# Optimization experiments

Measured on AMD Instinct MI355X. Metric: run time of the kernel, lower is better.

The kernel has to match this reference:

```python
import jax, jax.numpy as jnp
import numpy as np

B, S, D, K, NS = 4, 2048, 768, 8192, 2
TAU = 1.0


def setup_inputs() -> dict:
    key = jax.random.key(0)
    k1, k2, k3, k4 = jax.random.split(key, 4)
    x = jax.random.normal(k1, (B, S, D), dtype=jnp.float32)
    w_codebook = jax.random.normal(k2, (K, D), dtype=jnp.float32) * (1.0 / np.sqrt(D))
    embeddings = jax.random.normal(k3, (K, D), dtype=jnp.float32)
    # standard Gumbel(0,1) noise, one draw per (token, sample, code)
    gumbel_noise = jax.random.gumbel(k4, (B, S, NS, K), dtype=jnp.float32)
    return {"x": x, "w_codebook": w_codebook, "embeddings": embeddings,
            "gumbel_noise": gumbel_noise, "num_samples": NS}


def reference(x, w_codebook, embeddings, gumbel_noise, num_samples):
    # logits = Linear(x) without bias: [B, S, K]
    logits = jnp.einsum('bsd,kd->bsk', x, w_codebook)
    # expand over num_samples and add Gumbel noise (F.gumbel_softmax, training)
    g = (logits[:, :, None, :] + gumbel_noise) / TAU          # [B, S, NS, K]
    y_soft = jax.nn.softmax(g, axis=-1)
    # hard one-hot with straight-through estimator (hard=True, hard_p=1.0)
    idx = jnp.argmax(y_soft, axis=-1)                          # [B, S, NS]
    y_hard = jax.nn.one_hot(idx, K, dtype=y_soft.dtype)
    indices = y_hard + y_soft - jax.lax.stop_gradient(y_soft)  # [B, S, NS, K]
    # one-hot matmul == gather of codebook rows
    emb = jnp.einsum('bsnk,kd->bsnd', indices, embeddings)     # [B, S, NS, D]
    return emb, indices
```

## Files before the change

### kernel.cpp

```cpp
#include <hip/hip_runtime.h>
#include <stdint.h>

#define Bc 4
#define Sc 2048
#define Dc 768
#define Kc 8192
#define NSc 2
#define Mc (Bc*Sc)
#define EMB_ELEMS ((size_t)Mc*NSc*Dc)

typedef __attribute__((ext_vector_type(8))) __bf16 bf16x8;
typedef __attribute__((ext_vector_type(4))) float f32x4;
typedef __attribute__((ext_vector_type(4))) unsigned short u16x4;
typedef __attribute__((ext_vector_type(8))) unsigned short u16x8;

__device__ __forceinline__ unsigned short f2bf(float f){
  unsigned int u = __float_as_uint(f);
  u += 0x7FFFu + ((u >> 16) & 1u);
  return (unsigned short)(u >> 16);
}
__device__ __forceinline__ float bf2f(unsigned short h){
  return __uint_as_float(((unsigned int)h) << 16);
}

__global__ __launch_bounds__(256) void k_convert(const float4* __restrict__ x,
                                                 const float4* __restrict__ w,
                                                 u16x4* __restrict__ xb,
                                                 u16x4* __restrict__ wb){
  int i = blockIdx.x * 256 + threadIdx.x;
  float4 v = x[i];
  u16x4 o;
  o.x = f2bf(v.x); o.y = f2bf(v.y); o.z = f2bf(v.z); o.w = f2bf(v.w);
  xb[i] = o;
  v = w[i];
  o.x = f2bf(v.x); o.y = f2bf(v.y); o.z = f2bf(v.z); o.w = f2bf(v.w);
  wb[i] = o;
}

#define BM 128
#define BN 128
#define BK 32

__global__ __launch_bounds__(512, 2) void k_gemm(const unsigned short* __restrict__ xb,
                                                 const unsigned short* __restrict__ wb,
                                                 unsigned short* __restrict__ stash){
  __shared__ __align__(16) unsigned char lds[131072];

  const int tid  = threadIdx.x;
  const int lane = tid & 63;
  const int wid  = tid >> 6;
  const int wr   = wid >> 2;
  const int wc   = wid & 3;
  const int fr   = lane & 15;
  const int fq   = lane >> 4;

  const int bid = (int)blockIdx.x;
  const int xcd = bid & 7;
  const int ii  = bid >> 3;
  const int bm0 = (ii >> 2) * 256;
  const int bn0 = (xcd * 4 + (ii & 3)) * 256;

  f32x4 acc[8][4] = {};

  const int rin   = tid >> 3;
  const int kblkp = (tid & 7) ^ (rin & 7);
  const unsigned short* gsrc[8];
  unsigned dstoff[8];
  #pragma unroll
  for (int s = 0; s < 8; ++s) {
    const int isA = s >> 2;
    const int q   = s & 3;
    const int r64 = isA ? (((q & 1) << 1) | (q >> 1)) : q;
    const int grow = (isA ? bm0 : bn0) + r64 * 64 + rin;
    gsrc[s]   = (isA ? xb : wb) + (size_t)grow * Dc + kblkp * 8;
    dstoff[s] = (isA ? 0u : 32768u) + (unsigned)r64 * 8192u + (unsigned)wid * 1024u;
  }

#define ISSUE(s_, bo_) __builtin_amdgcn_global_load_lds( \
    (const __attribute__((address_space(1))) void*)gsrc[s_], \
    (__attribute__((address_space(3))) void*)&lds[(bo_) + dstoff[s_]], 16, 0, 0)

  #pragma unroll
  for (int s = 0; s < 8; ++s) ISSUE(s, 0u);
  #pragma unroll
  for (int s = 0; s < 8; ++s) gsrc[s] += 64;

  unsigned bufR = 0u, bufW = 65536u;
  const unsigned aRow = (unsigned)(wr*128 + fr) * 128u;
  const unsigned bRow = (unsigned)(wc*64  + fr) * 128u + 32768u;
  const unsigned sl0  = (unsigned)((fq       ) ^ (fr & 7)) * 16u;
  const unsigned sl1  = (unsigned)((fq + 4   ) ^ (fr & 7)) * 16u;

  for (int t = 0; t < 12; ++t) {
    const bool more = (t < 11);
    bf16x8 a[4], b0[4], b1[4];

    asm volatile("s_waitcnt vmcnt(2)" ::: "memory");
    __builtin_amdgcn_s_barrier();
    asm volatile("" ::: "memory");
    if (more) { ISSUE(0, bufW); ISSUE(1, bufW); }
    #pragma unroll
    for (int n = 0; n < 4; ++n) b0[n] = *(const bf16x8*)&lds[bufR + bRow + (unsigned)n*2048u + sl0];
    #pragma unroll
    for (int m = 0; m < 4; ++m) a[m]  = *(const bf16x8*)&lds[bufR + aRow + (unsigned)m*2048u + sl0];
    __builtin_amdgcn_s_setprio(1);
    #pragma unroll
    for (int m = 0; m < 4; ++m)
      #pragma unroll
      for (int n = 0; n < 4; ++n)
        acc[m][n] = __builtin_amdgcn_mfma_f32_16x16x32_bf16(a[m], b0[n], acc[m][n], 0, 0, 0);
    __builtin_amdgcn_s_setprio(0);

    if (more) asm volatile("s_waitcnt vmcnt(2)" ::: "memory");
    else      asm volatile("s_waitcnt vmcnt(0)" ::: "memory");
    __builtin_amdgcn_s_barrier();
    asm volatile("" ::: "memory");
    if (more) { ISSUE(2, bufW); ISSUE(3, bufW); }
    #pragma unroll
    for (int m = 0; m < 4; ++m) a[m] = *(const bf16x8*)&lds[bufR + aRow + 8192u + (unsigned)m*2048u + sl0];
    __builtin_amdgcn_s_setprio(1);
    #pragma unroll
    for (int m = 0; m < 4; ++m)
      #pragma unroll
      for (int n = 0; n < 4; ++n)
        acc[4+m][n] = __builtin_amdgcn_mfma_f32_16x16x32_bf16(a[m], b0[n], acc[4+m][n], 0, 0, 0);
    __builtin_amdgcn_s_setprio(0);

    if (more) { ISSUE(4, bufW); ISSUE(5, bufW); }
    #pragma unroll
    for (int n = 0; n < 4; ++n) b1[n] = *(const bf16x8*)&lds[bufR + bRow + (unsigned)n*2048u + sl1];
    #pragma unroll
    for (int m = 0; m < 4; ++m) a[m]  = *(const bf16x8*)&lds[bufR + aRow + (unsigned)m*2048u + sl1];
    __builtin_amdgcn_s_setprio(1);
    #pragma unroll
    for (int m = 0; m < 4; ++m)
      #pragma unroll
      for (int n = 0; n < 4; ++n)
        acc[m][n] = __builtin_amdgcn_mfma_f32_16x16x32_bf16(a[m], b1[n], acc[m][n], 0, 0, 0);
    __builtin_amdgcn_s_setprio(0);

    if (more) { ISSUE(6, bufW); ISSUE(7, bufW); }
    #pragma unroll
    for (int m = 0; m < 4; ++m) a[m] = *(const bf16x8*)&lds[bufR + aRow + 8192u + (unsigned)m*2048u + sl1];
    __builtin_amdgcn_s_setprio(1);
    #pragma unroll
    for (int m = 0; m < 4; ++m)
      #pragma unroll
      for (int n = 0; n < 4; ++n)
        acc[4+m][n] = __builtin_amdgcn_mfma_f32_16x16x32_bf16(a[m], b1[n], acc[4+m][n], 0, 0, 0);
    __builtin_amdgcn_s_setprio(0);

    bufR ^= 65536u; bufW ^= 65536u;
    if (t < 10) {
      #pragma unroll
      for (int s = 0; s < 8; ++s) gsrc[s] += 64;
    }
  }
#undef ISSUE

  unsigned short* tb16 = (unsigned short*)lds;
  #pragma unroll
  for (int h = 0; h < 2; ++h) {
    __syncthreads();
    if (wr == h) {
      #pragma unroll
      for (int m = 0; m < 8; ++m)
        #pragma unroll
        for (int n = 0; n < 4; ++n)
          #pragma unroll
          for (int r = 0; r < 4; ++r)
            tb16[(m*16 + fq*4 + r)*264 + (wc*64 + n*16 + fr)] = f2bf(acc[m][n][r]);
    }
    __syncthreads();
    #pragma unroll
    for (int i = 0; i < 8; ++i) {
      const int n = i*512 + tid;
      const int row = n >> 5, seg = n & 31;
      *(u16x8*)&stash[(size_t)(bm0 + h*128 + row) * 32768 + bn0 + seg*8] =
          *(const u16x8*)&tb16[row*264 + seg*8];
    }
  }
}

#define MARGIN 0.125f

__global__ __launch_bounds__(256) void k_select(const unsigned short* logits,
                                                const float* __restrict__ gumbel,
                                                const float* __restrict__ x,
                                                const float* __restrict__ w,
                                                const float* __restrict__ emb_tab,
                                                float* __restrict__ out_emb,
                                                float* out_ind){
  const int t   = blockIdx.x;
  const int tid = threadIdx.x;
  const int lane = tid & 63, wid = tid >> 6;

  __shared__ unsigned short Lrow[Kc];
  __shared__ float wmax[4];
  __shared__ int   cand_k[16];
  __shared__ float cand_g[16];
  __shared__ int   cand_cnt;
  __shared__ int   sel_idx[NSc];

  {
    const u16x4* src = (const u16x4*)(logits + (size_t)t * 32768);
    u16x4* dst = (u16x4*)Lrow;
    #pragma unroll
    for (int j = 0; j < 8; j++) dst[j*256 + tid] = src[j*256 + tid];
  }
  __syncthreads();

  for (int s = 0; s < NSc; ++s) {
    const float* grow = gumbel + ((size_t)t * NSc + s) * Kc;
    float4 vals[8];
    float m = -1e30f;
    #pragma unroll
    for (int j = 0; j < 8; j++) {
      float4 g4 = ((const float4*)grow)[j*256 + tid];
      u16x4 l4 = *(const u16x4*)&Lrow[j*1024 + tid*4];
      float4 v;
      v.x = bf2f(l4.x) + g4.x;
      v.y = bf2f(l4.y) + g4.y;
      v.z = bf2f(l4.z) + g4.z;
      v.w = bf2f(l4.w) + g4.w;
      vals[j] = v;
      m = fmaxf(m, fmaxf(fmaxf(v.x, v.y), fmaxf(v.z, v.w)));
    }
    #pragma unroll
    for (int off = 32; off; off >>= 1) m = fmaxf(m, __shfl_xor(m, off));
    if (lane == 0) wmax[wid] = m;
    __syncthreads();
    const float gmax = fmaxf(fmaxf(wmax[0], wmax[1]), fmaxf(wmax[2], wmax[3]));
    if (tid == 0) cand_cnt = 0;
    __syncthreads();

    const float thr = gmax - MARGIN;
    #pragma unroll
    for (int j = 0; j < 8; j++) {
      const int k0 = j*1024 + tid*4;
      float vv[4] = {vals[j].x, vals[j].y, vals[j].z, vals[j].w};
      #pragma unroll
      for (int q = 0; q < 4; q++) {
        if (vv[q] >= thr) {
          int p = atomicAdd(&cand_cnt, 1);
          if (p < 16) cand_k[p] = k0 + q;
        }
      }
    }
    __syncthreads();

    const int cnt = min(cand_cnt, 16);
    int idx;
    if (cnt == 1) {
      idx = cand_k[0];
    } else {
      for (int c = wid; c < cnt; c += 4) {
        const int kc = cand_k[c];
        const float* wr = w + (size_t)kc * Dc;
        const float* xr = x + (size_t)t * Dc;
        double accd = 0.0;
        for (int d = lane; d < Dc; d += 64) accd += (double)xr[d] * (double)wr[d];
        #pragma unroll
        for (int off = 32; off; off >>= 1) accd += __shfl_xor(accd, off);
        if (lane == 0) cand_g[c] = (float)accd + grow[kc];
      }
      __syncthreads();
      if (tid == 0) {
        float bg = -1e30f; int bk_ = Kc;
        for (int c = 0; c < cnt; c++) {
          float g = cand_g[c]; int kk = cand_k[c];
          if (g > bg || (g == bg && kk < bk_)) { bg = g; bk_ = kk; }
        }
        sel_idx[s] = bk_;
      }
      __syncthreads();
      idx = sel_idx[s];
    }
    if (cnt == 1 && tid == 0) sel_idx[s] = idx;
    __syncthreads();

    float* irow = out_ind + ((size_t)t * NSc + s) * Kc;
    #pragma unroll
    for (int j = 0; j < 8; j++) {
      const int k0 = j*1024 + tid*4;
      float4 z = {0.f, 0.f, 0.f, 0.f};
      const int d = sel_idx[s] - k0;
      if (d == 0) z.x = 1.0f; else if (d == 1) z.y = 1.0f;
      else if (d == 2) z.z = 1.0f; else if (d == 3) z.w = 1.0f;
      ((float4*)irow)[j*256 + tid] = z;
    }
    const float* er = emb_tab + (size_t)sel_idx[s] * Dc;
    float* eo = out_emb + ((size_t)t * NSc + s) * Dc;
    for (int d = tid; d < Dc; d += 256) eo[d] = er[d];
    __syncthreads();
  }
}

extern "C" void kernel_launch(void* const* d_in, const int* in_sizes, int n_in,
                              void* d_out, int out_size, void* d_ws, size_t ws_size,
                              hipStream_t stream) {
  const float* x   = (const float*)d_in[0];
  const float* w   = (const float*)d_in[1];
  const float* emb = (const float*)d_in[2];
  const float* gum = (const float*)d_in[3];

  float* out_emb = (float*)d_out;
  float* out_ind = out_emb + EMB_ELEMS;
  unsigned short* stash = (unsigned short*)out_ind;

  unsigned short* xb = (unsigned short*)d_ws;
  unsigned short* wb = xb + (size_t)Mc * Dc;

  const int n4 = (Mc * Dc) / 4;
  k_convert<<<n4 / 256, 256, 0, stream>>>((const float4*)x, (const float4*)w,
                                          (u16x4*)xb, (u16x4*)wb);
  k_gemm<<<1024, 512, 0, stream>>>(xb, wb, stash);
  k_select<<<Mc, 256, 0, stream>>>(stash, gum, x, w, emb, out_emb, out_ind);
}
```

Baseline: 374.3 us.

## Overlap zero-fill of one-hot output with GEMM main loop

Moves most zero-filling of the one-hot indices output into the GEMM kernel as nontemporal stores interleaved with the K loop, with waitcnt counts adjusted for the extra outstanding stores. The sampling kernel then only zeroes the part of each row that is not covered by the GEMM-stage stores, and places the two 1.0 entries afterwards. The aim is to hide output write bandwidth behind MFMA compute. It risks contending with the stash region of the same buffer, which the GEMM uses for bf16 logits, so the zeroed ranges must not overlap it. The waitcnt tuning also has to stay correct.

```diff
diff --git a/kernel.cpp b/kernel.cpp
--- a/kernel.cpp
+++ b/kernel.cpp
@@ -43,7 +43,7 @@
 
 __global__ __launch_bounds__(512, 2) void k_gemm(const unsigned short* __restrict__ xb,
                                                  const unsigned short* __restrict__ wb,
-                                                 unsigned short* __restrict__ stash){
+                                                 unsigned short* stash){
   __shared__ __align__(16) unsigned char lds[131072];
 
   const int tid  = threadIdx.x;
@@ -60,6 +60,9 @@
   const int bm0 = (ii >> 2) * 256;
   const int bn0 = (xcd * 4 + (ii & 3)) * 256;
 
+  float* zbase = (float*)stash;
+  const int zpan = bn0 >> 8;
+
   f32x4 acc[8][4] = {};
 
   const int rin   = tid >> 3;
@@ -80,6 +83,14 @@
     (const __attribute__((address_space(1))) void*)gsrc[s_], \
     (__attribute__((address_space(3))) void*)&lds[(bo_) + dstoff[s_]], 16, 0, 0)
 
+#define ZSTORE(u_) do { \
+    const unsigned g_ = (unsigned)(t*4 + (u_))*512u + (unsigned)tid; \
+    const unsigned tl_ = g_ / 96u, j4_ = g_ - tl_*96u; \
+    const f32x4 z_ = {0.f, 0.f, 0.f, 0.f}; \
+    __builtin_nontemporal_store(z_, (f32x4*)(zbase + \
+        (size_t)(bm0 + tl_)*16384 + 4096 + zpan*384 + j4_*4)); \
+  } while (0)
+
   #pragma unroll
   for (int s = 0; s < 8; ++s) ISSUE(s, 0u);
   #pragma unroll
@@ -95,7 +106,8 @@
     const bool more = (t < 11);
     bf16x8 a[4], b0[4], b1[4];
 
-    asm volatile("s_waitcnt vmcnt(2)" ::: "memory");
+    if (t == 0) asm volatile("s_waitcnt vmcnt(2)" ::: "memory");
+    else        asm volatile("s_waitcnt vmcnt(6)" ::: "memory");
     __builtin_amdgcn_s_barrier();
     asm volatile("" ::: "memory");
     if (more) { ISSUE(0, bufW); ISSUE(1, bufW); }
@@ -111,8 +123,9 @@
         acc[m][n] = __builtin_amdgcn_mfma_f32_16x16x32_bf16(a[m], b0[n], acc[m][n], 0, 0, 0);
     __builtin_amdgcn_s_setprio(0);
 
-    if (more) asm volatile("s_waitcnt vmcnt(2)" ::: "memory");
-    else      asm volatile("s_waitcnt vmcnt(0)" ::: "memory");
+    if (!more)      asm volatile("s_waitcnt vmcnt(0)" ::: "memory");
+    else if (t == 0) asm volatile("s_waitcnt vmcnt(2)" ::: "memory");
+    else            asm volatile("s_waitcnt vmcnt(4)" ::: "memory");
     __builtin_amdgcn_s_barrier();
     asm volatile("" ::: "memory");
     if (more) { ISSUE(2, bufW); ISSUE(3, bufW); }
@@ -127,6 +140,9 @@
     __builtin_amdgcn_s_setprio(0);
 
     if (more) { ISSUE(4, bufW); ISSUE(5, bufW); }
+    asm volatile("" ::: "memory");
+    ZSTORE(0); ZSTORE(1);
+    asm volatile("" ::: "memory");
     #pragma unroll
     for (int n = 0; n < 4; ++n) b1[n] = *(const bf16x8*)&lds[bufR + bRow + (unsigned)n*2048u + sl1];
     #pragma unroll
@@ -140,6 +156,9 @@
     __builtin_amdgcn_s_setprio(0);
 
     if (more) { ISSUE(6, bufW); ISSUE(7, bufW); }
+    asm volatile("" ::: "memory");
+    ZSTORE(2); ZSTORE(3);
+    asm volatile("" ::: "memory");
     #pragma unroll
     for (int m = 0; m < 4; ++m) a[m] = *(const bf16x8*)&lds[bufR + aRow + 8192u + (unsigned)m*2048u + sl1];
     __builtin_amdgcn_s_setprio(1);
@@ -156,6 +175,7 @@
       for (int s = 0; s < 8; ++s) gsrc[s] += 64;
     }
   }
+#undef ZSTORE
 #undef ISSUE
 
   unsigned short* tb16 = (unsigned short*)lds;
@@ -250,9 +270,8 @@
     __syncthreads();
 
     const int cnt = min(cand_cnt, 16);
-    int idx;
     if (cnt == 1) {
-      idx = cand_k[0];
+      if (tid == 0) sel_idx[s] = cand_k[0];
     } else {
       for (int c = wid; c < cnt; c += 4) {
         const int kc = cand_k[c];
@@ -273,26 +292,28 @@
         }
         sel_idx[s] = bk_;
       }
-      __syncthreads();
-      idx = sel_idx[s];
-    }
-    if (cnt == 1 && tid == 0) sel_idx[s] = idx;
-    __syncthreads();
-
-    float* irow = out_ind + ((size_t)t * NSc + s) * Kc;
-    #pragma unroll
-    for (int j = 0; j < 8; j++) {
-      const int k0 = j*1024 + tid*4;
-      float4 z = {0.f, 0.f, 0.f, 0.f};
-      const int d = sel_idx[s] - k0;
-      if (d == 0) z.x = 1.0f; else if (d == 1) z.y = 1.0f;
-      else if (d == 2) z.z = 1.0f; else if (d == 3) z.w = 1.0f;
-      ((float4*)irow)[j*256 + tid] = z;
-    }
+    }
+    __syncthreads();
+  }
+
+  {
+    float* row0lo = out_ind + (size_t)t * 16384;
+    const float4 z = {0.f, 0.f, 0.f, 0.f};
+    #pragma unroll
+    for (int q = 0; q < 4; ++q)
+      ((float4*)row0lo)[q*256 + tid] = z;
+  }
+  __syncthreads();
+  if (tid == 0) {
+    out_ind[(size_t)t*16384 +        sel_idx[0]] = 1.0f;
+    out_ind[(size_t)t*16384 + 8192 + sel_idx[1]] = 1.0f;
+  }
+
+  #pragma unroll
+  for (int s = 0; s < NSc; ++s) {
     const float* er = emb_tab + (size_t)sel_idx[s] * Dc;
-    float* eo = out_emb + ((size_t)t * NSc + s) * Dc;
+    float* eo = out_emb + ((size_t)t*NSc + s)*Dc;
     for (int d = tid; d < Dc; d += 256) eo[d] = er[d];
-    __syncthreads();
   }
 }
 
```

Measured after the change: 332.2 us. 11.2% less time.
